# Kernel tuning notes

Hardware: AMD Instinct MI355X
Metric: run time of the kernel (lower is better)

The kernel has to match this reference:

```python
import jax, jax.numpy as jnp
import numpy as np

N, D, H, L, E, G, C = 50000, 128, 128, 5, 800000, 512, 10


def setup_inputs() -> dict:
    key = jax.random.key(0)
    ks = jax.random.split(key, 16)
    s = 0.1  # normal init std (Weight_Initializer == 3 style; any init is fine for a math baseline)
    return {
        "x": jax.random.normal(ks[0], (N, D), jnp.float32),
        "edge_index": jax.random.randint(ks[1], (2, E), 0, N, jnp.int32),
        "edge_mask": jax.random.uniform(ks[2], (E,), jnp.float32),
        "batch": jnp.sort(jax.random.randint(ks[3], (N,), 0, G, jnp.int32)),
        "num_graphs": G,
        "eps": jnp.zeros((L,), jnp.float32),
        # per-GIN-layer 2-layer MLP (num_slp_layers=2): D -> H -> D, weights stored [in, out]
        "mlp_w1": jax.random.normal(ks[4], (L, D, H), jnp.float32) * s,
        "mlp_b1": jnp.zeros((L, H), jnp.float32),
        "mlp_w2": jax.random.normal(ks[5], (L, H, D), jnp.float32) * s,
        "mlp_b2": jnp.zeros((L, D), jnp.float32),
        # classifier head: lin1 [(L+1)*D -> (L+1)*D], lin2 [(L+1)*D -> C]
        "lin1_w": jax.random.normal(ks[6], ((L + 1) * D, (L + 1) * D), jnp.float32) * s,
        "lin1_b": jnp.zeros(((L + 1) * D,), jnp.float32),
        "lin2_w": jax.random.normal(ks[7], ((L + 1) * D, C), jnp.float32) * s,
        "lin2_b": jnp.zeros((C,), jnp.float32),
    }


def reference(x, edge_index, edge_mask, batch, num_graphs, eps,
              mlp_w1, mlp_b1, mlp_w2, mlp_b2, lin1_w, lin1_b, lin2_w, lin2_b):
    n = x.shape[0]
    src, dst = edge_index[0], edge_index[1]
    embeds = [x]
    h = x
    for l in range(eps.shape[0]):
        # A @ h with A[src,dst] = edge_mask: gather neighbor feats, weight, scatter-add to src
        agg = jax.ops.segment_sum(edge_mask[:, None] * h[dst], src, num_segments=n)  # [N,D]
        pooled = agg + (1.0 + eps[l]) * h
        h1 = jax.nn.relu(pooled @ mlp_w1[l] + mlp_b1[l])
        h = jax.nn.relu(h1 @ mlp_w2[l] + mlp_b2[l])
        embeds.append(h)
    stacked = jnp.stack(embeds)  # [L+1, N, D]
    # global_add_pool per layer, then per-graph concat across layers -> [G, (L+1)*D]
    pooled_g = jax.vmap(lambda e: jax.ops.segment_sum(e, batch, num_segments=num_graphs))(stacked)
    merged = jnp.transpose(pooled_g, (1, 0, 2)).reshape(num_graphs, -1)
    lin1_out = jax.nn.relu(merged @ lin1_w + lin1_b)  # dropout p=0 -> identity
    lin2_out = lin1_out @ lin2_w + lin2_b
    return jax.nn.softmax(lin2_out, axis=1)  # [G, C]
```

## Files before the change

kernel.cpp:

```cpp
#include <hip/hip_runtime.h>


typedef __bf16 bf16x8 __attribute__((ext_vector_type(8)));
typedef float f32x4 __attribute__((ext_vector_type(4)));

static inline int ceil_div(int a, int b) { return (a + b - 1) / b; }

__device__ inline ushort bf_rne(float v) {
  unsigned u = __float_as_uint(v);
  return (ushort)((u + 0x7fffu + ((u >> 16) & 1u)) >> 16);
}
__device__ inline float bf2f(ushort u) { return __uint_as_float((unsigned)u << 16); }
__device__ inline float bf2f_lo(unsigned g) { return __uint_as_float(g << 16); }
__device__ inline float bf2f_hi(unsigned g) { return __uint_as_float(g & 0xffff0000u); }

__global__ void k_hist(const int* __restrict__ src, int* __restrict__ deg, int E) {
  int i = blockIdx.x * blockDim.x + threadIdx.x;
  if (i < E) atomicAdd(&deg[src[i]], 1);
}

__global__ __launch_bounds__(256) void k_scan1(const int* __restrict__ deg,
                                               int* __restrict__ excl,
                                               int* __restrict__ bsum, int N) {
  __shared__ int tsum[256];
  int b = blockIdx.x, t = threadIdx.x;
  int base = b * 1024 + t * 4;
  int v0 = 0, v1 = 0, v2 = 0, v3 = 0;
  if (base + 3 < N) {
    int4 q = *(const int4*)&deg[base];
    v0 = q.x; v1 = q.y; v2 = q.z; v3 = q.w;
  } else {
    if (base + 0 < N) v0 = deg[base + 0];
    if (base + 1 < N) v1 = deg[base + 1];
    if (base + 2 < N) v2 = deg[base + 2];
    if (base + 3 < N) v3 = deg[base + 3];
  }
  tsum[t] = v0 + v1 + v2 + v3;
  __syncthreads();
  for (int off = 1; off < 256; off <<= 1) {
    int x = (t >= off) ? tsum[t - off] : 0;
    __syncthreads();
    tsum[t] += x;
    __syncthreads();
  }
  int pre = (t == 0) ? 0 : tsum[t - 1];
  if (base < N)     excl[base]     = pre;
  if (base + 1 < N) excl[base + 1] = pre + v0;
  if (base + 2 < N) excl[base + 2] = pre + v0 + v1;
  if (base + 3 < N) excl[base + 3] = pre + v0 + v1 + v2;
  if (t == 255) bsum[b] = tsum[255];
}

__global__ __launch_bounds__(256) void k_scan3(const int* __restrict__ excl,
                                               const int* __restrict__ bsum, int nb,
                                               int* __restrict__ rowptr,
                                               int* __restrict__ cursor, int N) {
  __shared__ int s[256];
  int t = threadIdx.x;
  s[t] = (t < nb) ? bsum[t] : 0;
  __syncthreads();
  for (int off = 1; off < 256; off <<= 1) {
    int x = (t >= off) ? s[t - off] : 0;
    __syncthreads();
    s[t] += x;
    __syncthreads();
  }
  int i = blockIdx.x * 256 + t;
  if (i < N) {
    int blk = i >> 10;
    int boff = blk ? s[blk - 1] : 0;
    int v = excl[i] + boff;
    rowptr[i] = v;
    cursor[i] = v;
  }
  if (i == N - 1) rowptr[N] = s[nb - 1];
}

__global__ void k_scatter(const int* __restrict__ src, const int* __restrict__ dst,
                          const float* __restrict__ mask, int* __restrict__ cursor,
                          int2* __restrict__ sedge, int E) {
  int i = blockIdx.x * blockDim.x + threadIdx.x;
  if (i < E) {
    int s = src[i];
    int p = atomicAdd(&cursor[s], 1);
    sedge[p] = make_int2(dst[i], __float_as_int(mask[i]));
  }
}

__global__ __launch_bounds__(256) void k_tobf16(const float* __restrict__ in,
                                                ushort* __restrict__ out, int n) {
  int base = (blockIdx.x * 256 + threadIdx.x) * 4;
  if (base + 3 < n) {
    float4 v = *(const float4*)&in[base];
    ushort4 o;
    o.x = bf_rne(v.x); o.y = bf_rne(v.y); o.z = bf_rne(v.z); o.w = bf_rne(v.w);
    *(ushort4*)&out[base] = o;
  } else {
    for (int k = base; k < n; ++k) out[k] = bf_rne(in[k]);
  }
}

__global__ __launch_bounds__(256) void k_prepw12(const float* __restrict__ W1,
                                                 const float* __restrict__ W2,
                                                 ushort* __restrict__ hi1,
                                                 ushort* __restrict__ hi2, int L) {
  __shared__ float t[32][33];
  int z = blockIdx.z;
  const float* Wm = (z < L) ? (W1 + (size_t)z * 128 * 128)
                            : (W2 + (size_t)(z - L) * 128 * 128);
  ushort* him = (z < L) ? (hi1 + (size_t)z * 128 * 128)
                        : (hi2 + (size_t)(z - L) * 128 * 128);
  int k0 = blockIdx.x * 32, n0 = blockIdx.y * 32;
  int tx = threadIdx.x & 31, ty = threadIdx.x >> 5;
#pragma unroll
  for (int r = 0; r < 32; r += 8)
    t[ty + r][tx] = Wm[(size_t)(k0 + ty + r) * 128 + n0 + tx];
  __syncthreads();
#pragma unroll
  for (int r = 0; r < 32; r += 8) {
    float v = t[tx][ty + r];
    him[(size_t)(n0 + ty + r) * 128 + k0 + tx] = bf_rne(v);
  }
}

__global__ __launch_bounds__(256) void k_prepw(const float* __restrict__ W,
                                               ushort* __restrict__ hi,
                                               ushort* __restrict__ lo,
                                               int K, int N) {
  __shared__ float t[32][33];
  int k0 = blockIdx.x * 32, n0 = blockIdx.y * 32;
  int tx = threadIdx.x & 31, ty = threadIdx.x >> 5;
#pragma unroll
  for (int r = 0; r < 32; r += 8)
    t[ty + r][tx] = W[(size_t)(k0 + ty + r) * N + n0 + tx];
  __syncthreads();
#pragma unroll
  for (int r = 0; r < 32; r += 8) {
    float v = t[tx][ty + r];
    size_t o = (size_t)(n0 + ty + r) * K + k0 + tx;
    ushort h = bf_rne(v);
    hi[o] = h;
    lo[o] = bf_rne(v - bf2f(h));
  }
}

__global__ __launch_bounds__(128) void k_agg(const ushort* __restrict__ h,
                                             const int* __restrict__ rowptr,
                                             const int2* __restrict__ sedge,
                                             const float* __restrict__ eps, int layer,
                                             ushort* __restrict__ pooled, int N) {
  int v = blockIdx.x * 2 + (threadIdx.x >> 6);
  int lane = threadIdx.x & 63;
  if (v >= N) return;
  int beg = rowptr[v], end = rowptr[v + 1];
  float ax[8] = {}, ay[8] = {};
  int j = beg;
  for (; j + 16 <= end; j += 16) {
    int2 e[16];
    unsigned g[16];
#pragma unroll
    for (int q = 0; q < 16; ++q) e[q] = sedge[j + q];
#pragma unroll
    for (int q = 0; q < 16; ++q)
      g[q] = *(const unsigned*)&h[(size_t)e[q].x * 128 + lane * 2];
#pragma unroll
    for (int q = 0; q < 16; ++q) {
      float m = __int_as_float(e[q].y);
      ax[q & 7] = fmaf(m, bf2f_lo(g[q]), ax[q & 7]);
      ay[q & 7] = fmaf(m, bf2f_hi(g[q]), ay[q & 7]);
    }
  }
  for (; j + 8 <= end; j += 8) {
    int2 e[8];
    unsigned g[8];
#pragma unroll
    for (int q = 0; q < 8; ++q) e[q] = sedge[j + q];
#pragma unroll
    for (int q = 0; q < 8; ++q)
      g[q] = *(const unsigned*)&h[(size_t)e[q].x * 128 + lane * 2];
#pragma unroll
    for (int q = 0; q < 8; ++q) {
      float m = __int_as_float(e[q].y);
      ax[q] = fmaf(m, bf2f_lo(g[q]), ax[q]);
      ay[q] = fmaf(m, bf2f_hi(g[q]), ay[q]);
    }
  }
  for (; j + 2 <= end; j += 2) {
    int2 e0 = sedge[j], e1 = sedge[j + 1];
    unsigned g0 = *(const unsigned*)&h[(size_t)e0.x * 128 + lane * 2];
    unsigned g1 = *(const unsigned*)&h[(size_t)e1.x * 128 + lane * 2];
    ax[0] = fmaf(__int_as_float(e0.y), bf2f_lo(g0), ax[0]);
    ay[0] = fmaf(__int_as_float(e0.y), bf2f_hi(g0), ay[0]);
    ax[1] = fmaf(__int_as_float(e1.y), bf2f_lo(g1), ax[1]);
    ay[1] = fmaf(__int_as_float(e1.y), bf2f_hi(g1), ay[1]);
  }
  if (j < end) {
    int2 e = sedge[j];
    unsigned g = *(const unsigned*)&h[(size_t)e.x * 128 + lane * 2];
    float m = __int_as_float(e.y);
    ax[0] = fmaf(m, bf2f_lo(g), ax[0]);
    ay[0] = fmaf(m, bf2f_hi(g), ay[0]);
  }
  float sx = ((ax[0] + ax[1]) + (ax[2] + ax[3])) + ((ax[4] + ax[5]) + (ax[6] + ax[7]));
  float sy = ((ay[0] + ay[1]) + (ay[2] + ay[3])) + ((ay[4] + ay[5]) + (ay[6] + ay[7]));
  float ep = 1.0f + eps[layer];
  unsigned gs = *(const unsigned*)&h[(size_t)v * 128 + lane * 2];
  sx = fmaf(ep, bf2f_lo(gs), sx);
  sy = fmaf(ep, bf2f_hi(gs), sy);
  unsigned outw = (unsigned)bf_rne(sx) | ((unsigned)bf_rne(sy) << 16);
  *(unsigned*)&pooled[(size_t)v * 128 + lane * 2] = outw;
}

__global__ __launch_bounds__(256) void k_mlp(
    const ushort* __restrict__ pooled,
    const ushort* __restrict__ w1t, const float* __restrict__ b1,
    const ushort* __restrict__ w2t, const float* __restrict__ b2,
    ushort* __restrict__ hout, int N) {
  __shared__ ushort Ws[128][128];
  __shared__ ushort H1s[64][128];
  int tid = threadIdx.x;
  int w = tid >> 6, lane = tid & 63;
  int row0 = blockIdx.x * 64;
  int wr = w >> 1, wc = w & 1;

#pragma unroll
  for (int i = 0; i < 8; ++i) {
    int f = i * 256 + tid;
    int r = f >> 4, c8 = (f & 15) * 8;
    *(bf16x8*)&Ws[r][c8 ^ ((r & 7) << 3)] = *(const bf16x8*)&w1t[(size_t)r * 128 + c8];
  }
  __syncthreads();

  f32x4 acc[2][4];
#pragma unroll
  for (int m = 0; m < 2; ++m)
#pragma unroll
    for (int n = 0; n < 4; ++n) acc[m][n] = (f32x4){0.f, 0.f, 0.f, 0.f};
#pragma unroll
  for (int ks = 0; ks < 4; ++ks) {
    int kk = ks * 32 + (lane >> 4) * 8;
    bf16x8 a[2], b[4];
#pragma unroll
    for (int m = 0; m < 2; ++m) {
      int arow = row0 + wr * 32 + m * 16 + (lane & 15);
      if (arow >= N) arow = N - 1;
      a[m] = *(const bf16x8*)&pooled[(size_t)arow * 128 + kk];
    }
#pragma unroll
    for (int n = 0; n < 4; ++n) {
      int r = wc * 64 + n * 16 + (lane & 15);
      b[n] = *(bf16x8*)&Ws[r][kk ^ ((r & 7) << 3)];
    }
#pragma unroll
    for (int m = 0; m < 2; ++m)
#pragma unroll
      for (int n = 0; n < 4; ++n)
        acc[m][n] = __builtin_amdgcn_mfma_f32_16x16x32_bf16(a[m], b[n], acc[m][n], 0, 0, 0);
  }
#pragma unroll
  for (int m = 0; m < 2; ++m) {
    int rbase = wr * 32 + m * 16 + (lane >> 4) * 4;
#pragma unroll
    for (int n = 0; n < 4; ++n) {
      int col = wc * 64 + n * 16 + (lane & 15);
      float bb = b1[col];
#pragma unroll
      for (int r = 0; r < 4; ++r) {
        int row = rbase + r;
        float v = fmaxf(acc[m][n][r] + bb, 0.f);
        H1s[row][col ^ ((row & 7) << 3)] = bf_rne(v);
      }
    }
  }
  __syncthreads();

#pragma unroll
  for (int i = 0; i < 8; ++i) {
    int f = i * 256 + tid;
    int r = f >> 4, c8 = (f & 15) * 8;
    *(bf16x8*)&Ws[r][c8 ^ ((r & 7) << 3)] = *(const bf16x8*)&w2t[(size_t)r * 128 + c8];
  }
  __syncthreads();

#pragma unroll
  for (int m = 0; m < 2; ++m)
#pragma unroll
    for (int n = 0; n < 4; ++n) acc[m][n] = (f32x4){0.f, 0.f, 0.f, 0.f};
#pragma unroll
  for (int ks = 0; ks < 4; ++ks) {
    int kk = ks * 32 + (lane >> 4) * 8;
    bf16x8 a[2], b[4];
#pragma unroll
    for (int m = 0; m < 2; ++m) {
      int r = wr * 32 + m * 16 + (lane & 15);
      a[m] = *(bf16x8*)&H1s[r][kk ^ ((r & 7) << 3)];
    }
#pragma unroll
    for (int n = 0; n < 4; ++n) {
      int r = wc * 64 + n * 16 + (lane & 15);
      b[n] = *(bf16x8*)&Ws[r][kk ^ ((r & 7) << 3)];
    }
#pragma unroll
    for (int m = 0; m < 2; ++m)
#pragma unroll
      for (int n = 0; n < 4; ++n)
        acc[m][n] = __builtin_amdgcn_mfma_f32_16x16x32_bf16(a[m], b[n], acc[m][n], 0, 0, 0);
  }
#pragma unroll
  for (int m = 0; m < 2; ++m) {
    int rbase = row0 + wr * 32 + m * 16 + (lane >> 4) * 4;
#pragma unroll
    for (int n = 0; n < 4; ++n) {
      int col = wc * 64 + n * 16 + (lane & 15);
      float bb = b2[col];
#pragma unroll
      for (int r = 0; r < 4; ++r) {
        int row = rbase + r;
        if (row < N) {
          float v = fmaxf(acc[m][n][r] + bb, 0.f);
          hout[(size_t)row * 128 + col] = bf_rne(v);
        }
      }
    }
  }
}

template <int RELU, int OUT_BF16, int SPLITW>
__global__ __launch_bounds__(256) void k_mgemm(const ushort* __restrict__ A,
                                               const ushort* __restrict__ Wt_hi,
                                               const ushort* __restrict__ Wt_lo,
                                               const float* __restrict__ bias,
                                               void* __restrict__ Cout,
                                               int M, int N, int K) {
  __shared__ ushort As[64][128];
  __shared__ ushort Ws_hi[64][128];
  __shared__ ushort Ws_lo[SPLITW ? 64 : 1][SPLITW ? 128 : 1];
  int tid = threadIdx.x;
  int row0 = blockIdx.y * 64, col0 = blockIdx.x * 64;
  int w = tid >> 6, lane = tid & 63;
  int wr = w >> 1, wc = w & 1;
  f32x4 acc[2][2] = {};
  int nk = K >> 7;
  for (int kc = 0; kc < nk; ++kc) {
    int k0 = kc << 7;
    if (kc) __syncthreads();
#pragma unroll
    for (int i = 0; i < 4; ++i) {
      int f = i * 256 + tid;
      int r = f >> 4, c8 = (f & 15) * 8;
      int ksw = c8 ^ ((r & 7) << 3);
      if (row0 + r < M) {
        *(bf16x8*)&As[r][ksw] = *(const bf16x8*)&A[(size_t)(row0 + r) * K + k0 + c8];
      } else {
        ushort4 z = {0, 0, 0, 0};
        *(ushort4*)&As[r][ksw] = z;
        *(ushort4*)&As[r][ksw + 4] = z;
      }
    }
#pragma unroll
    for (int i = 0; i < 4; ++i) {
      int f = i * 256 + tid;
      int r = f >> 4, c8 = (f & 15) * 8;
      int ksw = c8 ^ ((r & 7) << 3);
      *(bf16x8*)&Ws_hi[r][ksw] = *(const bf16x8*)&Wt_hi[(size_t)(col0 + r) * K + k0 + c8];
      if (SPLITW)
        *(bf16x8*)&Ws_lo[r][ksw] = *(const bf16x8*)&Wt_lo[(size_t)(col0 + r) * K + k0 + c8];
    }
    __syncthreads();
#pragma unroll
    for (int ks = 0; ks < 4; ++ks) {
      int kk = ks * 32 + (lane >> 4) * 8;
      bf16x8 a[2], bh[2], bl[2];
#pragma unroll
      for (int m = 0; m < 2; ++m) {
        int r = wr * 32 + m * 16 + (lane & 15);
        a[m] = *(bf16x8*)&As[r][kk ^ ((r & 7) << 3)];
      }
#pragma unroll
      for (int n = 0; n < 2; ++n) {
        int r = wc * 32 + n * 16 + (lane & 15);
        int ksw = kk ^ ((r & 7) << 3);
        bh[n] = *(bf16x8*)&Ws_hi[r][ksw];
        if (SPLITW) bl[n] = *(bf16x8*)&Ws_lo[r][ksw];
      }
#pragma unroll
      for (int m = 0; m < 2; ++m)
#pragma unroll
        for (int n = 0; n < 2; ++n) {
          acc[m][n] = __builtin_amdgcn_mfma_f32_16x16x32_bf16(a[m], bh[n], acc[m][n], 0, 0, 0);
          if (SPLITW)
            acc[m][n] = __builtin_amdgcn_mfma_f32_16x16x32_bf16(a[m], bl[n], acc[m][n], 0, 0, 0);
        }
    }
  }
#pragma unroll
  for (int m = 0; m < 2; ++m) {
    int rbase = row0 + wr * 32 + m * 16 + (lane >> 4) * 4;
#pragma unroll
    for (int n = 0; n < 2; ++n) {
      int col = col0 + wc * 32 + n * 16 + (lane & 15);
      float b = bias[col];
#pragma unroll
      for (int r = 0; r < 4; ++r) {
        int row = rbase + r;
        if (row < M) {
          float v = acc[m][n][r] + b;
          if (RELU) v = fmaxf(v, 0.f);
          if (OUT_BF16)
            ((ushort*)Cout)[(size_t)row * N + col] = bf_rne(v);
          else
            ((float*)Cout)[(size_t)row * N + col] = v;
        }
      }
    }
  }
}

__global__ __launch_bounds__(128) void k_pool_all(
    const ushort* __restrict__ f0, const ushort* __restrict__ f1,
    const ushort* __restrict__ f2, const ushort* __restrict__ f3,
    const ushort* __restrict__ f4, const ushort* __restrict__ f5,
    const int* __restrict__ batch, ushort* __restrict__ pg, int N, int L1) {
  __shared__ float red[2][64][2];
  int g = blockIdx.x;
  int slot = blockIdx.y;
  const ushort* feat;
  switch (slot) {
    case 0: feat = f0; break;
    case 1: feat = f1; break;
    case 2: feat = f2; break;
    case 3: feat = f3; break;
    case 4: feat = f4; break;
    default: feat = f5; break;
  }
  int w = threadIdx.x >> 6, lane = threadIdx.x & 63;
  int lo = 0, hi = N;
  while (lo < hi) {
    int mid = (lo + hi) >> 1;
    if (batch[mid] < g) lo = mid + 1; else hi = mid;
  }
  int s = lo;
  hi = N;
  while (lo < hi) {
    int mid = (lo + hi) >> 1;
    if (batch[mid] < g + 1) lo = mid + 1; else hi = mid;
  }
  int e = lo;
  float a0 = 0.f, a1 = 0.f;
#pragma unroll 4
  for (int v = s + w; v < e; v += 2) {
    unsigned u = *(const unsigned*)&feat[(size_t)v * 128 + lane * 2];
    a0 += bf2f_lo(u);
    a1 += bf2f_hi(u);
  }
  red[w][lane][0] = a0;
  red[w][lane][1] = a1;
  __syncthreads();
  if (w == 0) {
    a0 = red[0][lane][0] + red[1][lane][0];
    a1 = red[0][lane][1] + red[1][lane][1];
    unsigned outw = (unsigned)bf_rne(a0) | ((unsigned)bf_rne(a1) << 16);
    *(unsigned*)&pg[((size_t)g * L1 + slot) * 128 + lane * 2] = outw;
  }
}

__global__ __launch_bounds__(64) void k_lin2_softmax(const float* __restrict__ A,
                                                     const float* __restrict__ W,
                                                     const float* __restrict__ b,
                                                     float* __restrict__ out, int K, int C) {
  constexpr int CMAX = 16;
  int g = blockIdx.x;
  int lane = threadIdx.x;
  float acc[CMAX];
#pragma unroll
  for (int c = 0; c < CMAX; ++c) acc[c] = 0.f;
  for (int k = lane; k < K; k += 64) {
    float a = A[(size_t)g * K + k];
#pragma unroll
    for (int c = 0; c < CMAX; ++c)
      if (c < C) acc[c] = fmaf(a, W[(size_t)k * C + c], acc[c]);
  }
#pragma unroll
  for (int off = 32; off; off >>= 1)
#pragma unroll
    for (int c = 0; c < CMAX; ++c) acc[c] += __shfl_xor(acc[c], off, 64);
  if (lane == 0) {
    float mx = -3.0e38f;
#pragma unroll
    for (int c = 0; c < CMAX; ++c)
      if (c < C) {
        acc[c] += b[c];
        mx = fmaxf(mx, acc[c]);
      }
    float sum = 0.f;
#pragma unroll
    for (int c = 0; c < CMAX; ++c)
      if (c < C) {
        acc[c] = expf(acc[c] - mx);
        sum += acc[c];
      }
    float inv = 1.f / sum;
#pragma unroll
    for (int c = 0; c < CMAX; ++c)
      if (c < C) out[(size_t)g * C + c] = acc[c] * inv;
  }
}

extern "C" void kernel_launch(void* const* d_in, const int* in_sizes, int n_in,
                              void* d_out, int out_size, void* d_ws, size_t ws_size,
                              hipStream_t stream) {
  const float* x     = (const float*)d_in[0];
  const int*   eidx  = (const int*)d_in[1];
  const float* emask = (const float*)d_in[2];
  const int*   batch = (const int*)d_in[3];
  const float* eps   = (const float*)d_in[5];
  const float* w1    = (const float*)d_in[6];
  const float* b1    = (const float*)d_in[7];
  const float* w2    = (const float*)d_in[8];
  const float* b2    = (const float*)d_in[9];
  const float* l1w   = (const float*)d_in[10];
  const float* l1b   = (const float*)d_in[11];
  const float* l2w   = (const float*)d_in[12];
  const float* l2b   = (const float*)d_in[13];

  const int N = in_sizes[3];
  const int E = in_sizes[2];
  const int L = in_sizes[5];
  const int D = in_sizes[0] / N;
  const int C = in_sizes[13];
  const int G = out_size / C;
  const int L1 = L + 1;
  const int H = in_sizes[7] / L;
  const int F = L1 * D;

  const int* src = eidx;
  const int* dst = eidx + E;

  char* p = (char*)d_ws;
  auto carve = [&](size_t bytes) -> void* {
    void* r = (void*)p;
    p += (bytes + 255) & ~(size_t)255;
    return r;
  };
  int*    rowptr = (int*)carve((size_t)(N + 1) * 4);
  int*    cursor = (int*)carve((size_t)N * 4);
  int*    deg    = (int*)carve((size_t)N * 4);
  int*    excl   = (int*)carve((size_t)N * 4);
  int*    bsum   = (int*)carve(256 * 4);
  int2*   sedge  = (int2*)carve((size_t)E * 8);
  ushort* xb     = (ushort*)carve((size_t)N * D * 2);
  ushort* pooled = (ushort*)carve((size_t)N * D * 2);
  ushort* hb[5];
  for (int l = 0; l < 5; ++l) hb[l] = (ushort*)carve((size_t)N * D * 2);
  ushort* pg     = (ushort*)carve((size_t)G * F * 2);
  float*  l1out  = (float*)carve((size_t)G * F * 4);
  ushort* w1t_hi = (ushort*)carve((size_t)L * D * H * 2);
  ushort* w2t_hi = (ushort*)carve((size_t)L * H * D * 2);
  ushort* l1t_hi = (ushort*)carve((size_t)F * F * 2);
  ushort* l1t_lo = (ushort*)carve((size_t)F * F * 2);
  (void)ws_size;

  const int nb = ceil_div(N, 1024);
  hipMemsetAsync(deg, 0, (size_t)N * 4, stream);
  k_hist<<<ceil_div(E, 256), 256, 0, stream>>>(src, deg, E);
  k_scan1<<<nb, 256, 0, stream>>>(deg, excl, bsum, N);
  k_scan3<<<ceil_div(N, 256), 256, 0, stream>>>(excl, bsum, nb, rowptr, cursor, N);
  k_scatter<<<ceil_div(E, 256), 256, 0, stream>>>(src, dst, emask, cursor, sedge, E);

  k_tobf16<<<ceil_div(N * D, 1024), 256, 0, stream>>>(x, xb, N * D);
  k_prepw12<<<dim3(4, 4, 2 * L), 256, 0, stream>>>(w1, w2, w1t_hi, w2t_hi, L);
  k_prepw<<<dim3(F / 32, F / 32), 256, 0, stream>>>(l1w, l1t_hi, l1t_lo, F, F);

  const ushort* h_in = xb;
  for (int l = 0; l < L; ++l) {
    k_agg<<<ceil_div(N, 2), 128, 0, stream>>>(h_in, rowptr, sedge, eps, l, pooled, N);
    k_mlp<<<ceil_div(N, 64), 256, 0, stream>>>(
        pooled, w1t_hi + (size_t)l * D * H, b1 + (size_t)l * H,
        w2t_hi + (size_t)l * H * D, b2 + (size_t)l * D, hb[l], N);
    h_in = hb[l];
  }

  k_pool_all<<<dim3(G, L1), 128, 0, stream>>>(xb, hb[0], hb[1], hb[2], hb[3], hb[4],
                                              batch, pg, N, L1);

  k_mgemm<1, 0, 1><<<dim3(F / 64, ceil_div(G, 64)), 256, 0, stream>>>(
      pg, l1t_hi, l1t_lo, l1b, l1out, G, F, F);
  k_lin2_softmax<<<G, 64, 0, stream>>>(l1out, l2w, l2b, (float*)d_out, F, C);
}
```

Measured before the change: 421.9 us.

## Add nontemporal loads in aggregation, prefetch W2, merge weight-prep kernels

Several unrelated tweaks land together. The edge-list reads in aggregation and the feature reads in pooling become nontemporal loads, and the pooled output becomes a nontemporal store. The 16-wide unrolled gather loop is dropped in favour of the 8-wide one. The MLP kernel loads its second weight matrix into registers before the first GEMM, hiding that global latency at the cost of extra registers. The two weight-prep kernels are merged into one launch, which also schedules many blocks that exit immediately.

```diff
diff --git a/kernel.cpp b/kernel.cpp
--- a/kernel.cpp
+++ b/kernel.cpp
@@ -100,47 +100,42 @@
   }
 }
 
-__global__ __launch_bounds__(256) void k_prepw12(const float* __restrict__ W1,
-                                                 const float* __restrict__ W2,
-                                                 ushort* __restrict__ hi1,
-                                                 ushort* __restrict__ hi2, int L) {
+__global__ __launch_bounds__(256) void k_prep_all(
+    const float* __restrict__ W1, const float* __restrict__ W2,
+    const float* __restrict__ L1W,
+    ushort* __restrict__ hi1, ushort* __restrict__ hi2,
+    ushort* __restrict__ l1hi, ushort* __restrict__ l1lo, int L, int F) {
   __shared__ float t[32][33];
   int z = blockIdx.z;
-  const float* Wm = (z < L) ? (W1 + (size_t)z * 128 * 128)
-                            : (W2 + (size_t)(z - L) * 128 * 128);
-  ushort* him = (z < L) ? (hi1 + (size_t)z * 128 * 128)
-                        : (hi2 + (size_t)(z - L) * 128 * 128);
-  int k0 = blockIdx.x * 32, n0 = blockIdx.y * 32;
   int tx = threadIdx.x & 31, ty = threadIdx.x >> 5;
-#pragma unroll
-  for (int r = 0; r < 32; r += 8)
-    t[ty + r][tx] = Wm[(size_t)(k0 + ty + r) * 128 + n0 + tx];
-  __syncthreads();
-#pragma unroll
-  for (int r = 0; r < 32; r += 8) {
-    float v = t[tx][ty + r];
-    him[(size_t)(n0 + ty + r) * 128 + k0 + tx] = bf_rne(v);
-  }
-}
-
-__global__ __launch_bounds__(256) void k_prepw(const float* __restrict__ W,
-                                               ushort* __restrict__ hi,
-                                               ushort* __restrict__ lo,
-                                               int K, int N) {
-  __shared__ float t[32][33];
-  int k0 = blockIdx.x * 32, n0 = blockIdx.y * 32;
-  int tx = threadIdx.x & 31, ty = threadIdx.x >> 5;
-#pragma unroll
-  for (int r = 0; r < 32; r += 8)
-    t[ty + r][tx] = W[(size_t)(k0 + ty + r) * N + n0 + tx];
-  __syncthreads();
-#pragma unroll
-  for (int r = 0; r < 32; r += 8) {
-    float v = t[tx][ty + r];
-    size_t o = (size_t)(n0 + ty + r) * K + k0 + tx;
-    ushort h = bf_rne(v);
-    hi[o] = h;
-    lo[o] = bf_rne(v - bf2f(h));
+  if (z < 2 * L) {
+    if (blockIdx.x >= 4 || blockIdx.y >= 4) return;
+    const float* Wm = (z < L) ? (W1 + (size_t)z * 128 * 128)
+                              : (W2 + (size_t)(z - L) * 128 * 128);
+    ushort* him = (z < L) ? (hi1 + (size_t)z * 128 * 128)
+                          : (hi2 + (size_t)(z - L) * 128 * 128);
+    int k0 = blockIdx.x * 32, n0 = blockIdx.y * 32;
+#pragma unroll
+    for (int r = 0; r < 32; r += 8)
+      t[ty + r][tx] = Wm[(size_t)(k0 + ty + r) * 128 + n0 + tx];
+    __syncthreads();
+#pragma unroll
+    for (int r = 0; r < 32; r += 8)
+      him[(size_t)(n0 + ty + r) * 128 + k0 + tx] = bf_rne(t[tx][ty + r]);
+  } else {
+    int k0 = blockIdx.x * 32, n0 = blockIdx.y * 32;
+#pragma unroll
+    for (int r = 0; r < 32; r += 8)
+      t[ty + r][tx] = L1W[(size_t)(k0 + ty + r) * F + n0 + tx];
+    __syncthreads();
+#pragma unroll
+    for (int r = 0; r < 32; r += 8) {
+      float v = t[tx][ty + r];
+      size_t o = (size_t)(n0 + ty + r) * F + k0 + tx;
+      ushort h = bf_rne(v);
+      l1hi[o] = h;
+      l1lo[o] = bf_rne(v - bf2f(h));
+    }
   }
 }
 
@@ -155,49 +150,40 @@
   int beg = rowptr[v], end = rowptr[v + 1];
   float ax[8] = {}, ay[8] = {};
   int j = beg;
-  for (; j + 16 <= end; j += 16) {
-    int2 e[16];
-    unsigned g[16];
-#pragma unroll
-    for (int q = 0; q < 16; ++q) e[q] = sedge[j + q];
-#pragma unroll
-    for (int q = 0; q < 16; ++q)
-      g[q] = *(const unsigned*)&h[(size_t)e[q].x * 128 + lane * 2];
-#pragma unroll
-    for (int q = 0; q < 16; ++q) {
-      float m = __int_as_float(e[q].y);
-      ax[q & 7] = fmaf(m, bf2f_lo(g[q]), ax[q & 7]);
-      ay[q & 7] = fmaf(m, bf2f_hi(g[q]), ay[q & 7]);
-    }
-  }
   for (; j + 8 <= end; j += 8) {
-    int2 e[8];
+    long long e[8];
     unsigned g[8];
 #pragma unroll
-    for (int q = 0; q < 8; ++q) e[q] = sedge[j + q];
-#pragma unroll
     for (int q = 0; q < 8; ++q)
-      g[q] = *(const unsigned*)&h[(size_t)e[q].x * 128 + lane * 2];
+      e[q] = __builtin_nontemporal_load((const long long*)(sedge + j + q));
 #pragma unroll
     for (int q = 0; q < 8; ++q) {
-      float m = __int_as_float(e[q].y);
+      int d = (int)(unsigned)e[q];
+      g[q] = *(const unsigned*)&h[(size_t)d * 128 + lane * 2];
+    }
+#pragma unroll
+    for (int q = 0; q < 8; ++q) {
+      float m = __int_as_float((int)(e[q] >> 32));
       ax[q] = fmaf(m, bf2f_lo(g[q]), ax[q]);
       ay[q] = fmaf(m, bf2f_hi(g[q]), ay[q]);
     }
   }
   for (; j + 2 <= end; j += 2) {
-    int2 e0 = sedge[j], e1 = sedge[j + 1];
-    unsigned g0 = *(const unsigned*)&h[(size_t)e0.x * 128 + lane * 2];
-    unsigned g1 = *(const unsigned*)&h[(size_t)e1.x * 128 + lane * 2];
-    ax[0] = fmaf(__int_as_float(e0.y), bf2f_lo(g0), ax[0]);
-    ay[0] = fmaf(__int_as_float(e0.y), bf2f_hi(g0), ay[0]);
-    ax[1] = fmaf(__int_as_float(e1.y), bf2f_lo(g1), ax[1]);
-    ay[1] = fmaf(__int_as_float(e1.y), bf2f_hi(g1), ay[1]);
+    long long e0 = __builtin_nontemporal_load((const long long*)(sedge + j));
+    long long e1 = __builtin_nontemporal_load((const long long*)(sedge + j + 1));
+    unsigned g0 = *(const unsigned*)&h[(size_t)(int)(unsigned)e0 * 128 + lane * 2];
+    unsigned g1 = *(const unsigned*)&h[(size_t)(int)(unsigned)e1 * 128 + lane * 2];
+    float m0 = __int_as_float((int)(e0 >> 32));
+    float m1 = __int_as_float((int)(e1 >> 32));
+    ax[0] = fmaf(m0, bf2f_lo(g0), ax[0]);
+    ay[0] = fmaf(m0, bf2f_hi(g0), ay[0]);
+    ax[1] = fmaf(m1, bf2f_lo(g1), ax[1]);
+    ay[1] = fmaf(m1, bf2f_hi(g1), ay[1]);
   }
   if (j < end) {
-    int2 e = sedge[j];
-    unsigned g = *(const unsigned*)&h[(size_t)e.x * 128 + lane * 2];
-    float m = __int_as_float(e.y);
+    long long e = __builtin_nontemporal_load((const long long*)(sedge + j));
+    unsigned g = *(const unsigned*)&h[(size_t)(int)(unsigned)e * 128 + lane * 2];
+    float m = __int_as_float((int)(e >> 32));
     ax[0] = fmaf(m, bf2f_lo(g), ax[0]);
     ay[0] = fmaf(m, bf2f_hi(g), ay[0]);
   }
@@ -208,7 +194,7 @@
   sx = fmaf(ep, bf2f_lo(gs), sx);
   sy = fmaf(ep, bf2f_hi(gs), sy);
   unsigned outw = (unsigned)bf_rne(sx) | ((unsigned)bf_rne(sy) << 16);
-  *(unsigned*)&pooled[(size_t)v * 128 + lane * 2] = outw;
+  __builtin_nontemporal_store(outw, (unsigned*)&pooled[(size_t)v * 128 + lane * 2]);
 }
 
 __global__ __launch_bounds__(256) void k_mlp(
@@ -229,6 +215,13 @@
     int r = f >> 4, c8 = (f & 15) * 8;
     *(bf16x8*)&Ws[r][c8 ^ ((r & 7) << 3)] = *(const bf16x8*)&w1t[(size_t)r * 128 + c8];
   }
+  bf16x8 w2r[8];
+#pragma unroll
+  for (int i = 0; i < 8; ++i) {
+    int f = i * 256 + tid;
+    int r = f >> 4, c8 = (f & 15) * 8;
+    w2r[i] = *(const bf16x8*)&w2t[(size_t)r * 128 + c8];
+  }
   __syncthreads();
 
   f32x4 acc[2][4];
@@ -278,7 +271,7 @@
   for (int i = 0; i < 8; ++i) {
     int f = i * 256 + tid;
     int r = f >> 4, c8 = (f & 15) * 8;
-    *(bf16x8*)&Ws[r][c8 ^ ((r & 7) << 3)] = *(const bf16x8*)&w2t[(size_t)r * 128 + c8];
+    *(bf16x8*)&Ws[r][c8 ^ ((r & 7) << 3)] = w2r[i];
   }
   __syncthreads();
 
@@ -449,7 +442,7 @@
   float a0 = 0.f, a1 = 0.f;
 #pragma unroll 4
   for (int v = s + w; v < e; v += 2) {
-    unsigned u = *(const unsigned*)&feat[(size_t)v * 128 + lane * 2];
+    unsigned u = __builtin_nontemporal_load((const unsigned*)&feat[(size_t)v * 128 + lane * 2]);
     a0 += bf2f_lo(u);
     a1 += bf2f_hi(u);
   }
@@ -568,8 +561,8 @@
   k_scatter<<<ceil_div(E, 256), 256, 0, stream>>>(src, dst, emask, cursor, sedge, E);
 
   k_tobf16<<<ceil_div(N * D, 1024), 256, 0, stream>>>(x, xb, N * D);
-  k_prepw12<<<dim3(4, 4, 2 * L), 256, 0, stream>>>(w1, w2, w1t_hi, w2t_hi, L);
-  k_prepw<<<dim3(F / 32, F / 32), 256, 0, stream>>>(l1w, l1t_hi, l1t_lo, F, F);
+  k_prep_all<<<dim3(F / 32, F / 32, 2 * L + 1), 256, 0, stream>>>(
+      w1, w2, l1w, w1t_hi, w2t_hi, l1t_hi, l1t_lo, L, F);
 
   const ushort* h_in = xb;
   for (int l = 0; l < L; ++l) {
```

After: 459.7 us. 1.09x slower.
